# Kernel tuning notes

Measured on AMD Instinct MI355X. Metric: run time of the kernel, lower is better.

## Reference

```python
import jax, jax.numpy as jnp
import numpy as np

DEPTH = 10


def setup_inputs() -> dict:
    key = jax.random.key(0)
    k1, k2, k3, k4 = jax.random.split(key, 4)
    B, C_in, O, D, L = 4096, 512, 1024, DEPTH, 2 ** DEPTH
    x = jax.random.normal(k1, (B, C_in), dtype=jnp.float32)
    thresholds = 6.0 * jax.random.uniform(k2, (O, D), dtype=jnp.float32) - 3.0
    ordinals = jax.random.randint(k3, (O, D), 0, C_in, dtype=jnp.int64)
    weights = jax.random.normal(k4, (O, L), dtype=jnp.float32)
    return {"x": x, "thresholds": thresholds, "ordinals": ordinals, "weights": weights}


def reference(x, thresholds, ordinals, weights):
    # x: [B, C_in]; thresholds/ordinals: [O, D]; weights: [O, 2**D]
    O, D = thresholds.shape
    # Gather the D decision features for each fern: [B, O, D]
    feats = x[:, ordinals]
    margins = feats - thresholds[None, :, :]
    # Leaf index from sign bits (bit d is MSB-first): [B, O]
    powers = (2 ** (D - 1 - jnp.arange(D))).astype(jnp.int32)
    bits = (margins > 0).astype(jnp.int32)
    leaf = jnp.sum(bits * powers, axis=-1)
    # Hinge value: minimum absolute margin along the path: [B, O]
    min_margin = jnp.min(jnp.abs(margins), axis=-1)
    # Select leaf weight per (batch, fern): w[o, leaf[b, o]]
    w_sel = jnp.take_along_axis(weights[None, :, :], leaf[:, :, None], axis=2)[..., 0]
    return w_sel * min_margin  # [B, O]
```

## Files before the change

kernel.cpp:

```cpp
#include <hip/hip_runtime.h>


#define B_TOT  4096
#define CIN    512
#define O_TOT  1024
#define DEPTH  10
#define LEAVES 1024
#define BT     64
#define OT     64
#define NTHR   512

typedef float vf4 __attribute__((ext_vector_type(4)));

__global__ __launch_bounds__(NTHR, 2) void fern_kernel(
    const float* __restrict__ x,
    const float* __restrict__ thresholds,
    const int*   __restrict__ ordinals,
    const float* __restrict__ weights,
    float*       __restrict__ out)
{
    __shared__ float xT[CIN * BT];
    __shared__ float osh[BT * OT];

    const int t    = threadIdx.x;
    const int lane = t & 63;
    const int wu   = __builtin_amdgcn_readfirstlane(t >> 6);
    const int b0   = blockIdx.x * BT;
    const int o0   = blockIdx.y * OT;

#pragma unroll
    for (int k = 0; k < 16; ++k) {
        const int id = k * NTHR + t;
        const int r  = id >> 7;
        const int c4 = id & 127;
        const vf4 v = *reinterpret_cast<const vf4*>(
            x + (size_t)(b0 + r) * CIN + (c4 << 2));
        const int rs   = r ^ (c4 & 31);
        const int base = (c4 << 2) * BT + rs;
        xT[base]          = v.x;
        xT[base + BT]     = v.y;
        xT[base + 2 * BT] = v.z;
        xT[base + 3 * BT] = v.w;
    }
    __syncthreads();

#pragma unroll
    for (int i = 0; i < 8; ++i) {
        const int ol = wu * 8 + i;
        const int o  = o0 + ol;
        const int*   op = ordinals   + o * DEPTH;
        const float* tp = thresholds + o * DEPTH;

        int   leaf = 0;
        float mm   = 1e30f;
#pragma unroll
        for (int d = 0; d < DEPTH; ++d) {
            const int   ord = op[d];
            const float thr = tp[d];
            const float xv  = xT[ord * BT + (lane ^ ((ord >> 2) & 31))];
            const float mg  = xv - thr;
            leaf = (leaf << 1) | (mg > 0.0f ? 1 : 0);
            mm   = fminf(mm, fabsf(mg));
        }
        const float wv = weights[(size_t)o * LEAVES + leaf];
        osh[lane * OT + (ol ^ lane)] = wv * mm;
    }
    __syncthreads();

    const int rb = t >> 3;
#pragma unroll
    for (int k = 0; k < 2; ++k) {
        const int g  = (t & 7) + (k << 3);
        const int ob = g << 2;
        vf4 v;
        v.x = osh[rb * OT + ((ob + 0) ^ rb)];
        v.y = osh[rb * OT + ((ob + 1) ^ rb)];
        v.z = osh[rb * OT + ((ob + 2) ^ rb)];
        v.w = osh[rb * OT + ((ob + 3) ^ rb)];
        __builtin_nontemporal_store(v, reinterpret_cast<vf4*>(
            out + (size_t)(b0 + rb) * O_TOT + o0 + ob));
    }
}

extern "C" void kernel_launch(void* const* d_in, const int* in_sizes, int n_in,
                              void* d_out, int out_size, void* d_ws, size_t ws_size,
                              hipStream_t stream) {
    const float* x          = (const float*)d_in[0];
    const float* thresholds = (const float*)d_in[1];
    const int*   ordinals   = (const int*)d_in[2];
    const float* weights    = (const float*)d_in[3];
    float*       out        = (float*)d_out;

    dim3 grid(B_TOT / BT, O_TOT / OT);
    fern_kernel<<<grid, NTHR, 0, stream>>>(x, thresholds, ordinals, weights, out);
}
```

Measured before the change: 92.97 us.

## Pre-transpose x into workspace and gather features directly from global memory

Adds a separate transpose kernel that writes x as [C_in, B] into the workspace. The fern kernel then reads gathered features straight from global memory, with coalesced 64-lane rows per feature, instead of staging a 128KB transposed tile in LDS per block. Dropping that LDS tile removes the per-block reload of x and the LDS occupancy limit, and the block shrinks to 256 threads with more blocks per CU. In exchange it pays an extra kernel launch and a global round trip for xT, and the random feature gathers now depend on L2 hit rates.

```diff
diff --git a/kernel.cpp b/kernel.cpp
--- a/kernel.cpp
+++ b/kernel.cpp
@@ -6,47 +6,65 @@
 #define O_TOT  1024
 #define DEPTH  10
 #define LEAVES 1024
-#define BT     64
-#define OT     64
-#define NTHR   512
 
 typedef float vf4 __attribute__((ext_vector_type(4)));
 
-__global__ __launch_bounds__(NTHR, 2) void fern_kernel(
+__global__ __launch_bounds__(256, 4) void transpose_kernel(
     const float* __restrict__ x,
+    float* __restrict__ xT)
+{
+    __shared__ float tile[64 * 64];
+    const int t  = threadIdx.x;
+    const int c0 = blockIdx.x * 64;
+    const int r0 = blockIdx.y * 64;
+
+#pragma unroll
+    for (int k = 0; k < 4; ++k) {
+        const int id = k * 256 + t;
+        const int r  = id >> 4;
+        const int c4 = id & 15;
+        const vf4 v = *reinterpret_cast<const vf4*>(
+            x + (size_t)(r0 + r) * CIN + c0 + (c4 << 2));
+        const int c = c4 << 2;
+        tile[r * 64 + ((c + 0) ^ r)] = v.x;
+        tile[r * 64 + ((c + 1) ^ r)] = v.y;
+        tile[r * 64 + ((c + 2) ^ r)] = v.z;
+        tile[r * 64 + ((c + 3) ^ r)] = v.w;
+    }
+    __syncthreads();
+
+#pragma unroll
+    for (int k = 0; k < 4; ++k) {
+        const int id = k * 256 + t;
+        const int c  = id >> 4;
+        const int j4 = id & 15;
+        vf4 v;
+        v.x = tile[(j4 * 4 + 0) * 64 + (c ^ (j4 * 4 + 0))];
+        v.y = tile[(j4 * 4 + 1) * 64 + (c ^ (j4 * 4 + 1))];
+        v.z = tile[(j4 * 4 + 2) * 64 + (c ^ (j4 * 4 + 2))];
+        v.w = tile[(j4 * 4 + 3) * 64 + (c ^ (j4 * 4 + 3))];
+        *reinterpret_cast<vf4*>(xT + (size_t)(c0 + c) * B_TOT + r0 + (j4 << 2)) = v;
+    }
+}
+
+__global__ __launch_bounds__(256, 4) void fern_kernel(
+    const float* __restrict__ xT,
     const float* __restrict__ thresholds,
     const int*   __restrict__ ordinals,
     const float* __restrict__ weights,
     float*       __restrict__ out)
 {
-    __shared__ float xT[CIN * BT];
-    __shared__ float osh[BT * OT];
+    __shared__ float osh[64 * 64];
 
     const int t    = threadIdx.x;
     const int lane = t & 63;
     const int wu   = __builtin_amdgcn_readfirstlane(t >> 6);
-    const int b0   = blockIdx.x * BT;
-    const int o0   = blockIdx.y * OT;
+    const int b0   = blockIdx.x * 64;
+    const int o0   = blockIdx.y * 64;
 
-#pragma unroll
-    for (int k = 0; k < 16; ++k) {
-        const int id = k * NTHR + t;
-        const int r  = id >> 7;
-        const int c4 = id & 127;
-        const vf4 v = *reinterpret_cast<const vf4*>(
-            x + (size_t)(b0 + r) * CIN + (c4 << 2));
-        const int rs   = r ^ (c4 & 31);
-        const int base = (c4 << 2) * BT + rs;
-        xT[base]          = v.x;
-        xT[base + BT]     = v.y;
-        xT[base + 2 * BT] = v.z;
-        xT[base + 3 * BT] = v.w;
-    }
-    __syncthreads();
-
-#pragma unroll
-    for (int i = 0; i < 8; ++i) {
-        const int ol = wu * 8 + i;
+#pragma unroll 2
+    for (int i = 0; i < 16; ++i) {
+        const int ol = wu * 16 + i;
         const int o  = o0 + ol;
         const int*   op = ordinals   + o * DEPTH;
         const float* tp = thresholds + o * DEPTH;
@@ -56,27 +74,26 @@
 #pragma unroll
         for (int d = 0; d < DEPTH; ++d) {
             const int   ord = op[d];
-            const float thr = tp[d];
-            const float xv  = xT[ord * BT + (lane ^ ((ord >> 2) & 31))];
-            const float mg  = xv - thr;
+            const float xv  = xT[(size_t)ord * B_TOT + b0 + lane];
+            const float mg  = xv - tp[d];
             leaf = (leaf << 1) | (mg > 0.0f ? 1 : 0);
             mm   = fminf(mm, fabsf(mg));
         }
         const float wv = weights[(size_t)o * LEAVES + leaf];
-        osh[lane * OT + (ol ^ lane)] = wv * mm;
+        osh[lane * 64 + (ol ^ lane)] = wv * mm;
     }
     __syncthreads();
 
-    const int rb = t >> 3;
 #pragma unroll
-    for (int k = 0; k < 2; ++k) {
-        const int g  = (t & 7) + (k << 3);
-        const int ob = g << 2;
+    for (int k = 0; k < 4; ++k) {
+        const int id = k * 256 + t;
+        const int rb = id >> 4;
+        const int ob = (id & 15) << 2;
         vf4 v;
-        v.x = osh[rb * OT + ((ob + 0) ^ rb)];
-        v.y = osh[rb * OT + ((ob + 1) ^ rb)];
-        v.z = osh[rb * OT + ((ob + 2) ^ rb)];
-        v.w = osh[rb * OT + ((ob + 3) ^ rb)];
+        v.x = osh[rb * 64 + ((ob + 0) ^ rb)];
+        v.y = osh[rb * 64 + ((ob + 1) ^ rb)];
+        v.z = osh[rb * 64 + ((ob + 2) ^ rb)];
+        v.w = osh[rb * 64 + ((ob + 3) ^ rb)];
         __builtin_nontemporal_store(v, reinterpret_cast<vf4*>(
             out + (size_t)(b0 + rb) * O_TOT + o0 + ob));
     }
@@ -90,7 +107,11 @@
     const int*   ordinals   = (const int*)d_in[2];
     const float* weights    = (const float*)d_in[3];
     float*       out        = (float*)d_out;
+    float*       xT         = (float*)d_ws;
 
-    dim3 grid(B_TOT / BT, O_TOT / OT);
-    fern_kernel<<<grid, NTHR, 0, stream>>>(x, thresholds, ordinals, weights, out);
+    dim3 tg(CIN / 64, B_TOT / 64);
+    transpose_kernel<<<tg, 256, 0, stream>>>(x, xT);
+
+    dim3 fg(B_TOT / 64, O_TOT / 64);
+    fern_kernel<<<fg, 256, 0, stream>>>(xT, thresholds, ordinals, weights, out);
 }
```

Measured after the change: 93.12 us. Within noise of the previous version (+0.2%).
